# Optimization experiments

Measured on AMD Instinct MI355X. Metric: run time of the kernel, lower is better.

Reference implementation:

```python
import jax, jax.numpy as jnp
import numpy as np


def setup_inputs() -> dict:
    key = jax.random.key(0)
    ks = jax.random.split(key, 10)
    B, L, D_MODEL = 2, 2048, 1024
    D_INNER, N, W, R = 2048, 16, 4, 64
    s = 0.02
    return {
        "hidden_states": jax.random.normal(ks[0], (B, L, D_MODEL), jnp.float32),
        "in_proj_w": jax.random.normal(ks[1], (2 * D_INNER, D_MODEL), jnp.float32) * s,
        "conv_w": jax.random.normal(ks[2], (D_INNER, W), jnp.float32) * 0.2,
        "conv_b": jax.random.normal(ks[3], (D_INNER,), jnp.float32) * 0.02,
        "x_proj_w": jax.random.normal(ks[4], (R + 2 * N, D_INNER), jnp.float32) * s,
        "dt_proj_w": jax.random.normal(ks[5], (D_INNER, R), jnp.float32) * (R ** -0.5),
        "dt_proj_b": jnp.log(jnp.expm1(jnp.exp(jax.random.uniform(ks[6], (D_INNER,), jnp.float32, np.log(1e-3), np.log(1e-1)))) + 1e-20),
        "A_log": jnp.log(jnp.broadcast_to(jnp.arange(1, N + 1, dtype=jnp.float32), (D_INNER, N))),
        "D_param": jnp.ones((D_INNER,), jnp.float32),
        "out_proj_w": jax.random.normal(ks[7], (D_MODEL, D_INNER), jnp.float32) * s,
    }


def _mamba_fwd(hidden_states, in_proj_w, conv_w, conv_b, x_proj_w,
               dt_proj_w, dt_proj_b, A_log, D_param, out_proj_w):
    Bsz, L, _ = hidden_states.shape
    d_inner = conv_w.shape[0]
    n = A_log.shape[1]
    r = dt_proj_w.shape[1]

    # input projection -> x, z  (each [B, L, d_inner])
    xz = jnp.einsum('bld,ed->ble', hidden_states, in_proj_w)
    x, z = xz[..., :d_inner], xz[..., d_inner:]

    # depthwise causal conv over L with SiLU
    x_bdl = jnp.transpose(x, (0, 2, 1))  # [B, d, L]
    kern = conv_w[:, None, :]            # [d, 1, W]
    xc = jax.lax.conv_general_dilated(
        x_bdl, kern, window_strides=(1,), padding=[(conv_w.shape[1] - 1, 0)],
        dimension_numbers=('NCH', 'OIH', 'NCH'), feature_group_count=d_inner)
    xc = xc + conv_b[None, :, None]
    xc = xc * jax.nn.sigmoid(xc)         # silu, [B, d, L]
    u = jnp.transpose(xc, (0, 2, 1))     # [B, L, d]

    # SSM parameter projections
    x_dbl = jnp.einsum('bld,ed->ble', u, x_proj_w)   # [B, L, r+2n]
    dt_lo = x_dbl[..., :r]
    B_ssm = x_dbl[..., r:r + n]                       # [B, L, n]
    C_ssm = x_dbl[..., r + n:]                        # [B, L, n]
    delta = jax.nn.softplus(jnp.einsum('blr,dr->bld', dt_lo, dt_proj_w) + dt_proj_b)

    A = -jnp.exp(A_log)  # [d, n]

    # selective scan over time (sequential recurrence)
    def step(h, inp):
        d_t, u_t, b_t, c_t = inp  # [B,d], [B,d], [B,n], [B,n]
        dA = jnp.exp(d_t[..., None] * A)                       # [B,d,n]
        h = dA * h + (d_t * u_t)[..., None] * b_t[:, None, :]  # [B,d,n]
        y_t = jnp.einsum('bdn,bn->bd', h, c_t)
        return h, y_t

    h0 = jnp.zeros((Bsz, d_inner, n), dtype=u.dtype)
    xs = (jnp.transpose(delta, (1, 0, 2)), jnp.transpose(u, (1, 0, 2)),
          jnp.transpose(B_ssm, (1, 0, 2)), jnp.transpose(C_ssm, (1, 0, 2)))
    _, ys = jax.lax.scan(step, h0, xs)           # ys: [L, B, d]
    y = jnp.transpose(ys, (1, 0, 2)) + u * D_param
    y = y * (z * jax.nn.sigmoid(z))              # gate: y * silu(z)
    return jnp.einsum('bld,ed->ble', y, out_proj_w)


def reference(hidden_states, in_proj_w, conv_w, conv_b, x_proj_w,
              dt_proj_w, dt_proj_b, A_log, D_param, out_proj_w):
    return _mamba_fwd(hidden_states, in_proj_w, conv_w, conv_b, x_proj_w,
                      dt_proj_w, dt_proj_b, A_log, D_param, out_proj_w)
```

## Files before the change

### kernel.cpp

```cpp
#include <hip/hip_runtime.h>
#include <cstdint>
#include <cstddef>

#define Bsz  2
#define Lseq 2048
#define DM   1024
#define DI   2048
#define NS   16
#define RR   64
#define BL   (Bsz * Lseq)
#define TC   64
#define NC   (Lseq / TC)

typedef unsigned short u16;
typedef __attribute__((ext_vector_type(8))) short short8;
typedef __attribute__((ext_vector_type(4))) float f32x4;

__device__ __forceinline__ u16 f32_to_bf16(float f) {
  union { float f; unsigned int u; } v; v.f = f;
  unsigned int lsb = (v.u >> 16) & 1u;
  v.u += 0x7fffu + lsb;
  return (u16)(v.u >> 16);
}
__device__ __forceinline__ float bf16_to_f32(u16 h) {
  union { unsigned int u; float f; } v; v.u = ((unsigned int)h) << 16;
  return v.f;
}

__global__ void cvt_f32_bf16(const float* __restrict__ src, u16* __restrict__ dst, int n) {
  int i = (blockIdx.x * blockDim.x + threadIdx.x) * 4;
  if (i + 4 <= n) {
    float4 v = *(const float4*)(src + i);
    dst[i + 0] = f32_to_bf16(v.x);
    dst[i + 1] = f32_to_bf16(v.y);
    dst[i + 2] = f32_to_bf16(v.z);
    dst[i + 3] = f32_to_bf16(v.w);
  } else {
    for (; i < n; ++i) dst[i] = f32_to_bf16(src[i]);
  }
}

__global__ void split_bf16_kernel(const float* __restrict__ src,
                                  u16* __restrict__ hi, u16* __restrict__ lo, int n) {
  int i = blockIdx.x * blockDim.x + threadIdx.x;
  if (i >= n) return;
  const float v = src[i];
  const u16 h = f32_to_bf16(v);
  hi[i] = h;
  lo[i] = f32_to_bf16(v - bf16_to_f32(h));
}

__global__ void split_dt_kernel(const float* __restrict__ xdbl,
                                u16* __restrict__ hi, u16* __restrict__ lo) {
  int i = blockIdx.x * blockDim.x + threadIdx.x;
  if (i >= BL * 64) return;
  const int m = i >> 6, k = i & 63;
  const float v = xdbl[(size_t)m * 96 + k];
  const u16 h = f32_to_bf16(v);
  hi[i] = h;
  lo[i] = f32_to_bf16(v - bf16_to_f32(h));
}

__device__ __forceinline__ void gload_lds16(const u16* g, u16* l) {
  __builtin_amdgcn_global_load_lds(
      (const __attribute__((address_space(1))) unsigned int*)g,
      (__attribute__((address_space(3))) unsigned int*)l,
      16, 0, 0);
}

__global__ __launch_bounds__(256) void gemm128_bt(
    const u16* __restrict__ A, const u16* __restrict__ Bt,
    float* __restrict__ outA, float* __restrict__ outB,
    int split, int ldA, int ldB, int K)
{
  __shared__ __align__(16) u16 As[128 * 32];
  __shared__ __align__(16) u16 Bs[128 * 32];
  const int tid  = threadIdx.x;
  const int lane = tid & 63;
  const int wid  = tid >> 6;
  const int m0 = blockIdx.y * 128;
  const int n0 = blockIdx.x * 128;
  const int wr = wid >> 1, wc = wid & 1;

  const f32x4 zero = {0.f, 0.f, 0.f, 0.f};
  f32x4 acc[4][4];
#pragma unroll
  for (int i = 0; i < 4; ++i)
#pragma unroll
    for (int j = 0; j < 4; ++j) acc[i][j] = zero;

  const int l16 = lane * 16;

  for (int k0 = 0; k0 < K; k0 += 32) {
    __syncthreads();
#pragma unroll
    for (int c = 0; c < 2; ++c) {
      const int base = c * 4096 + wid * 1024;
      const int ofs  = base + l16;
      const int row  = ofs >> 6;
      const int col  = (ofs >> 1) & 31;
      gload_lds16(A  + (size_t)(m0 + row) * K + k0 + col, (u16*)((char*)As + base));
      gload_lds16(Bt + (size_t)(n0 + row) * K + k0 + col, (u16*)((char*)Bs + base));
    }
    __syncthreads();

    const int kk = (lane >> 4) * 8;
    const int ra = wr * 64 + (lane & 15);
    const int rb = wc * 64 + (lane & 15);
    short8 af[4], bf[4];
#pragma unroll
    for (int i = 0; i < 4; ++i) af[i] = *(const short8*)&As[(ra + i * 16) * 32 + kk];
#pragma unroll
    for (int j = 0; j < 4; ++j) bf[j] = *(const short8*)&Bs[(rb + j * 16) * 32 + kk];
#pragma unroll
    for (int i = 0; i < 4; ++i)
#pragma unroll
      for (int j = 0; j < 4; ++j)
        acc[i][j] = __builtin_amdgcn_mfma_f32_16x16x32_bf16(af[i], bf[j], acc[i][j], 0, 0, 0);
  }

  const int cr = (lane >> 4) * 4;
  const int cc = lane & 15;
#pragma unroll
  for (int i = 0; i < 4; ++i)
#pragma unroll
    for (int j = 0; j < 4; ++j)
#pragma unroll
      for (int r = 0; r < 4; ++r) {
        const int m = m0 + wr * 64 + i * 16 + cr + r;
        const int n = n0 + wc * 64 + j * 16 + cc;
        const float v = acc[i][j][r];
        if (n < split) outA[(size_t)m * ldA + n] = v;
        else           outB[(size_t)m * ldB + (n - split)] = v;
      }
}

__global__ __launch_bounds__(256) void gemm_wave16_bt(
    const u16* __restrict__ A, const u16* __restrict__ Bt,
    float* __restrict__ C, int M, int N, int K)
{
  const int wg   = blockIdx.x * 4 + (threadIdx.x >> 6);
  const int lane = threadIdx.x & 63;
  const int ntiles = N / 16;
  const int mt = wg / ntiles, nt = wg % ntiles;
  if (mt * 16 >= M) return;

  const u16* arow = A  + (size_t)(mt * 16 + (lane & 15)) * K + ((lane >> 4) * 8);
  const u16* brow = Bt + (size_t)(nt * 16 + (lane & 15)) * K + ((lane >> 4) * 8);
  f32x4 acc = {0.f, 0.f, 0.f, 0.f};
  for (int k0 = 0; k0 < K; k0 += 32) {
    short8 a = *(const short8*)(arow + k0);
    short8 b = *(const short8*)(brow + k0);
    acc = __builtin_amdgcn_mfma_f32_16x16x32_bf16(a, b, acc, 0, 0, 0);
  }
  const int cr = (lane >> 4) * 4, cc = lane & 15;
#pragma unroll
  for (int r = 0; r < 4; ++r)
    C[(size_t)(mt * 16 + cr + r) * N + nt * 16 + cc] = acc[r];
}

__global__ __launch_bounds__(256) void dt_gemm_mfma(
    const u16* __restrict__ ahi, const u16* __restrict__ alo,
    const u16* __restrict__ bhi, const u16* __restrict__ blo,
    const float* __restrict__ dtb, float* __restrict__ delta)
{
  const int wg   = blockIdx.x * 4 + (threadIdx.x >> 6);
  const int lane = threadIdx.x & 63;
  const int mt = wg >> 7, nt = wg & 127;

  const size_t aofs = (size_t)(mt * 16 + (lane & 15)) * 64 + ((lane >> 4) * 8);
  const size_t bofs = (size_t)(nt * 16 + (lane & 15)) * 64 + ((lane >> 4) * 8);

  f32x4 acc = {0.f, 0.f, 0.f, 0.f};
#pragma unroll
  for (int k0 = 0; k0 < 64; k0 += 32) {
    const short8 Ah = *(const short8*)(ahi + aofs + k0);
    const short8 Al = *(const short8*)(alo + aofs + k0);
    const short8 Bh = *(const short8*)(bhi + bofs + k0);
    const short8 Bl = *(const short8*)(blo + bofs + k0);
    acc = __builtin_amdgcn_mfma_f32_16x16x32_bf16(Ah, Bh, acc, 0, 0, 0);
    acc = __builtin_amdgcn_mfma_f32_16x16x32_bf16(Ah, Bl, acc, 0, 0, 0);
    acc = __builtin_amdgcn_mfma_f32_16x16x32_bf16(Al, Bh, acc, 0, 0, 0);
  }

  const int cr = (lane >> 4) * 4, cc = lane & 15;
  const int n  = nt * 16 + cc;
  const float b = dtb[n];
#pragma unroll
  for (int r = 0; r < 4; ++r) {
    const float s = acc[r] + b;
    const float sp = fmaxf(s, 0.f) + __logf(1.f + __expf(-fabsf(s)));
    delta[(size_t)(mt * 16 + cr + r) * DI + n] = sp;
  }
}

__global__ void conv_silu_kernel(const float* __restrict__ x,
                                 const float* __restrict__ cw, const float* __restrict__ cb,
                                 float* __restrict__ uf, u16* __restrict__ ub)
{
  const int idx = blockIdx.x * blockDim.x + threadIdx.x;
  if (idx >= BL * DI) return;
  const int d  = idx & (DI - 1);
  const int bl = idx >> 11;
  const int l  = bl & (Lseq - 1);
  const float4 w = *(const float4*)(cw + d * 4);
  float acc = cb[d];
  const float* xp = x + (size_t)bl * DI + d;
  const float x0 = (l >= 3) ? xp[-3 * DI] : 0.f;
  const float x1 = (l >= 2) ? xp[-2 * DI] : 0.f;
  const float x2 = (l >= 1) ? xp[-1 * DI] : 0.f;
  const float x3 = xp[0];
  acc += x0 * w.x + x1 * w.y + x2 * w.z + x3 * w.w;
  const float s = acc / (1.f + __expf(-acc));
  uf[idx] = s;
  ub[idx] = f32_to_bf16(s);
}


__global__ __launch_bounds__(256) void scan_chunk_ps(
    const float* __restrict__ delta, const float* __restrict__ u,
    const float* __restrict__ xdbl, const float* __restrict__ alog,
    float* __restrict__ Pout, float* __restrict__ Sout)
{
  __shared__ float Bl[TC][NS];
  const int b   = blockIdx.z;
  const int c   = blockIdx.y;
  const int d   = blockIdx.x * 256 + threadIdx.x;
  const int tid = threadIdx.x;
  const size_t rowBase = (size_t)b * Lseq + (size_t)c * TC;

  {
    const int row = tid >> 2, c4 = (tid & 3) * 4;
    *(float4*)&Bl[row][c4] = *(const float4*)&xdbl[(rowBase + row) * 96 + RR + c4];
  }
  __syncthreads();

  float A[NS];
#pragma unroll
  for (int n4 = 0; n4 < 4; ++n4) {
    const float4 a4 = *(const float4*)&alog[(size_t)d * NS + n4 * 4];
    A[n4 * 4 + 0] = -__expf(a4.x);
    A[n4 * 4 + 1] = -__expf(a4.y);
    A[n4 * 4 + 2] = -__expf(a4.z);
    A[n4 * 4 + 3] = -__expf(a4.w);
  }

  float h[NS], P[NS];
#pragma unroll
  for (int n = 0; n < NS; ++n) { h[n] = 0.f; P[n] = 1.f; }

#pragma unroll 4
  for (int t = 0; t < TC; ++t) {
    const float dt  = delta[(rowBase + t) * DI + d];
    const float ut  = u[(rowBase + t) * DI + d];
    const float dtu = dt * ut;
#pragma unroll
    for (int n = 0; n < NS; ++n) {
      const float dA = __expf(dt * A[n]);
      P[n] *= dA;
      h[n] = dA * h[n] + dtu * Bl[t][n];
    }
  }

  const size_t base = (size_t)(b * NC + c) * NS * DI + d;
#pragma unroll
  for (int n = 0; n < NS; ++n) {
    Pout[base + (size_t)n * DI] = P[n];
    Sout[base + (size_t)n * DI] = h[n];
  }
}

__global__ __launch_bounds__(256) void scan_combine(
    const float* __restrict__ P, const float* __restrict__ S,
    float* __restrict__ Hin)
{
  const int gid = blockIdx.x * 256 + threadIdx.x;
  const int b   = gid >> 15;
  const int nd  = gid & 32767;
  float h = 0.f;
  for (int c = 0; c < NC; ++c) {
    const size_t o = (size_t)(b * NC + c) * (NS * DI) + nd;
    const float Pc = P[o];
    const float Sc = S[o];
    Hin[o] = h;
    h = Pc * h + Sc;
  }
}

__global__ __launch_bounds__(256) void scan_chunk_y(
    const float* __restrict__ delta, const float* __restrict__ u,
    const float* __restrict__ xdbl, const float* __restrict__ alog,
    const float* __restrict__ dpar, const float* __restrict__ z,
    const float* __restrict__ Hin, u16* __restrict__ yb)
{
  __shared__ float Bl[TC][NS];
  __shared__ float Cl[TC][NS];
  const int b   = blockIdx.z;
  const int c   = blockIdx.y;
  const int d   = blockIdx.x * 256 + threadIdx.x;
  const int tid = threadIdx.x;
  const size_t rowBase = (size_t)b * Lseq + (size_t)c * TC;

  {
    const int row = tid >> 2, c4 = (tid & 3) * 4;
    *(float4*)&Bl[row][c4] = *(const float4*)&xdbl[(rowBase + row) * 96 + RR + c4];
    *(float4*)&Cl[row][c4] = *(const float4*)&xdbl[(rowBase + row) * 96 + RR + NS + c4];
  }
  __syncthreads();

  float A[NS];
#pragma unroll
  for (int n4 = 0; n4 < 4; ++n4) {
    const float4 a4 = *(const float4*)&alog[(size_t)d * NS + n4 * 4];
    A[n4 * 4 + 0] = -__expf(a4.x);
    A[n4 * 4 + 1] = -__expf(a4.y);
    A[n4 * 4 + 2] = -__expf(a4.z);
    A[n4 * 4 + 3] = -__expf(a4.w);
  }
  const float Dv = dpar[d];

  float h[NS];
  const size_t sbase = (size_t)(b * NC + c) * NS * DI + d;
#pragma unroll
  for (int n = 0; n < NS; ++n) h[n] = Hin[sbase + (size_t)n * DI];

#pragma unroll 4
  for (int t = 0; t < TC; ++t) {
    const float dt  = delta[(rowBase + t) * DI + d];
    const float ut  = u[(rowBase + t) * DI + d];
    const float zv  = z[(rowBase + t) * DI + d];
    const float dtu = dt * ut;
    float y = 0.f;
#pragma unroll
    for (int n = 0; n < NS; ++n) {
      const float dA = __expf(dt * A[n]);
      h[n] = dA * h[n] + dtu * Bl[t][n];
      y += h[n] * Cl[t][n];
    }
    const float yv = y + ut * Dv;
    const float g  = zv / (1.f + __expf(-zv));
    yb[(rowBase + t) * DI + d] = f32_to_bf16(yv * g);
  }
}

extern "C" void kernel_launch(void* const* d_in, const int* in_sizes, int n_in,
                              void* d_out, int out_size, void* d_ws, size_t ws_size,
                              hipStream_t stream)
{
  const float* hs   = (const float*)d_in[0];
  const float* win  = (const float*)d_in[1];
  const float* cw   = (const float*)d_in[2];
  const float* cb   = (const float*)d_in[3];
  const float* wxp  = (const float*)d_in[4];
  const float* wdt  = (const float*)d_in[5];
  const float* bdt  = (const float*)d_in[6];
  const float* alog = (const float*)d_in[7];
  const float* dpar = (const float*)d_in[8];
  const float* wout = (const float*)d_in[9];
  float* out = (float*)d_out;

  char* ws = (char*)d_ws;
  size_t off = 0;
  auto alloc = [&](size_t bytes) -> void* {
    void* p = ws + off;
    off += (bytes + 255) & ~(size_t)255;
    return p;
  };
  u16*   hs_b   = (u16*)  alloc((size_t)BL * DM * 2);
  u16*   win_b  = (u16*)  alloc((size_t)2 * DI * DM * 2);
  u16*   wxp_b  = (u16*)  alloc((size_t)96 * DI * 2);
  u16*   wout_b = (u16*)  alloc((size_t)DM * DI * 2);
  float* xbuf   = (float*)alloc((size_t)BL * DI * 4);
  float* zbuf   = (float*)alloc((size_t)BL * DI * 4);
  float* ubuf   = (float*)alloc((size_t)BL * DI * 4);
  u16*   ub16   = (u16*)  alloc((size_t)BL * DI * 2);
  float* xdbl   = (float*)alloc((size_t)BL * 96 * 4);
  float* Pbuf   = (float*)alloc((size_t)Bsz * NC * DI * NS * 4);
  float* Sbuf   = (float*)alloc((size_t)Bsz * NC * DI * NS * 4);
  u16*   dt_hi  = (u16*)  alloc((size_t)BL * 64 * 2);
  u16*   dt_lo  = (u16*)  alloc((size_t)BL * 64 * 2);
  u16*   w_hi   = (u16*)  alloc((size_t)DI * 64 * 2);
  u16*   w_lo   = (u16*)  alloc((size_t)DI * 64 * 2);
  float* deltab = xbuf;
  u16*   y_b    = ub16;
  float* Hin    = Pbuf;

  const int thr = 256;
  cvt_f32_bf16<<<(BL * DM / 4 + thr - 1) / thr, thr, 0, stream>>>(hs, hs_b, BL * DM);
  cvt_f32_bf16<<<(2 * DI * DM / 4 + thr - 1) / thr, thr, 0, stream>>>(win, win_b, 2 * DI * DM);
  cvt_f32_bf16<<<(96 * DI / 4 + thr - 1) / thr, thr, 0, stream>>>(wxp, wxp_b, 96 * DI);
  cvt_f32_bf16<<<(DM * DI / 4 + thr - 1) / thr, thr, 0, stream>>>(wout, wout_b, DM * DI);
  split_bf16_kernel<<<(DI * 64) / thr, thr, 0, stream>>>(wdt, w_hi, w_lo, DI * 64);

  {
    dim3 g(4096 / 128, BL / 128);
    gemm128_bt<<<g, 256, 0, stream>>>(hs_b, win_b, xbuf, zbuf, DI, DI, DI, DM);
  }

  conv_silu_kernel<<<(BL * DI) / 256, 256, 0, stream>>>(xbuf, cw, cb, ubuf, ub16);

  gemm_wave16_bt<<<(BL / 16) * (96 / 16) / 4, 256, 0, stream>>>(ub16, wxp_b, xdbl, BL, 96, DI);

  split_dt_kernel<<<(BL * 64) / thr, thr, 0, stream>>>(xdbl, dt_hi, dt_lo);
  dt_gemm_mfma<<<(256 * 128) / 4, 256, 0, stream>>>(dt_hi, dt_lo, w_hi, w_lo, bdt, deltab);

  {
    dim3 gA(DI / 256, NC, Bsz);
    scan_chunk_ps<<<gA, 256, 0, stream>>>(deltab, ubuf, xdbl, alog, Pbuf, Sbuf);
    scan_combine<<<(Bsz * DI * NS) / 256, 256, 0, stream>>>(Pbuf, Sbuf, Hin);
    scan_chunk_y<<<gA, 256, 0, stream>>>(deltab, ubuf, xdbl, alog, dpar, zbuf, Hin, y_b);
  }

  {
    dim3 g(DM / 128, BL / 128);
    gemm128_bt<<<g, 256, 0, stream>>>(y_b, wout_b, out, out, DM, DM, DM, DI);
  }
}
```

Measured before the change: 294.3 us.

## Store x/z/u intermediates in bf16 and fuse dt split into x_proj GEMM

The input projection GEMM now writes x and z as bf16 instead of fp32. The conv kernel reads bf16 and is vectorised four channels per thread, producing only a bf16 u buffer. Both scan kernels read u and z as bf16. The x_proj GEMM epilogue now does the hi/lo bf16 split for the dt columns, which removes the separate split kernel and a launch. This roughly halves the global traffic for the large BL×DI intermediates, at the cost of lower precision in u, z and the pre-conv x, which may affect accuracy tolerance.

```diff
diff --git a/kernel.cpp b/kernel.cpp
--- a/kernel.cpp
+++ b/kernel.cpp
@@ -13,6 +13,7 @@
 #define NC   (Lseq / TC)
 
 typedef unsigned short u16;
+typedef __attribute__((ext_vector_type(4))) unsigned short u16x4;
 typedef __attribute__((ext_vector_type(8))) short short8;
 typedef __attribute__((ext_vector_type(4))) float f32x4;
 
@@ -50,17 +51,6 @@
   lo[i] = f32_to_bf16(v - bf16_to_f32(h));
 }
 
-__global__ void split_dt_kernel(const float* __restrict__ xdbl,
-                                u16* __restrict__ hi, u16* __restrict__ lo) {
-  int i = blockIdx.x * blockDim.x + threadIdx.x;
-  if (i >= BL * 64) return;
-  const int m = i >> 6, k = i & 63;
-  const float v = xdbl[(size_t)m * 96 + k];
-  const u16 h = f32_to_bf16(v);
-  hi[i] = h;
-  lo[i] = f32_to_bf16(v - bf16_to_f32(h));
-}
-
 __device__ __forceinline__ void gload_lds16(const u16* g, u16* l) {
   __builtin_amdgcn_global_load_lds(
       (const __attribute__((address_space(1))) unsigned int*)g,
@@ -68,9 +58,10 @@
       16, 0, 0);
 }
 
+template<bool BF16OUT>
 __global__ __launch_bounds__(256) void gemm128_bt(
     const u16* __restrict__ A, const u16* __restrict__ Bt,
-    float* __restrict__ outA, float* __restrict__ outB,
+    void* __restrict__ outA_, void* __restrict__ outB_,
     int split, int ldA, int ldB, int K)
 {
   __shared__ __align__(16) u16 As[128 * 32];
@@ -130,33 +121,49 @@
         const int m = m0 + wr * 64 + i * 16 + cr + r;
         const int n = n0 + wc * 64 + j * 16 + cc;
         const float v = acc[i][j][r];
-        if (n < split) outA[(size_t)m * ldA + n] = v;
-        else           outB[(size_t)m * ldB + (n - split)] = v;
+        const bool isA = (n < split);
+        const int  nn  = isA ? n : n - split;
+        const int  ld  = isA ? ldA : ldB;
+        if constexpr (BF16OUT) {
+          u16* o = isA ? (u16*)outA_ : (u16*)outB_;
+          o[(size_t)m * ld + nn] = f32_to_bf16(v);
+        } else {
+          float* o = isA ? (float*)outA_ : (float*)outB_;
+          o[(size_t)m * ld + nn] = v;
+        }
       }
 }
 
-__global__ __launch_bounds__(256) void gemm_wave16_bt(
+__global__ __launch_bounds__(256) void gemm_xproj(
     const u16* __restrict__ A, const u16* __restrict__ Bt,
-    float* __restrict__ C, int M, int N, int K)
+    float* __restrict__ xdbl, u16* __restrict__ dhi, u16* __restrict__ dlo)
 {
   const int wg   = blockIdx.x * 4 + (threadIdx.x >> 6);
   const int lane = threadIdx.x & 63;
-  const int ntiles = N / 16;
-  const int mt = wg / ntiles, nt = wg % ntiles;
-  if (mt * 16 >= M) return;
-
-  const u16* arow = A  + (size_t)(mt * 16 + (lane & 15)) * K + ((lane >> 4) * 8);
-  const u16* brow = Bt + (size_t)(nt * 16 + (lane & 15)) * K + ((lane >> 4) * 8);
+  const int mt = wg / 6, nt = wg % 6;
+
+  const u16* arow = A  + (size_t)(mt * 16 + (lane & 15)) * DI + ((lane >> 4) * 8);
+  const u16* brow = Bt + (size_t)(nt * 16 + (lane & 15)) * DI + ((lane >> 4) * 8);
   f32x4 acc = {0.f, 0.f, 0.f, 0.f};
-  for (int k0 = 0; k0 < K; k0 += 32) {
+  for (int k0 = 0; k0 < DI; k0 += 32) {
     short8 a = *(const short8*)(arow + k0);
     short8 b = *(const short8*)(brow + k0);
     acc = __builtin_amdgcn_mfma_f32_16x16x32_bf16(a, b, acc, 0, 0, 0);
   }
   const int cr = (lane >> 4) * 4, cc = lane & 15;
-#pragma unroll
-  for (int r = 0; r < 4; ++r)
-    C[(size_t)(mt * 16 + cr + r) * N + nt * 16 + cc] = acc[r];
+  const int n  = nt * 16 + cc;
+#pragma unroll
+  for (int r = 0; r < 4; ++r) {
+    const int m = mt * 16 + cr + r;
+    const float v = acc[r];
+    if (n < RR) {
+      const u16 h = f32_to_bf16(v);
+      dhi[(size_t)m * RR + n] = h;
+      dlo[(size_t)m * RR + n] = f32_to_bf16(v - bf16_to_f32(h));
+    } else {
+      xdbl[(size_t)m * 96 + n] = v;
+    }
+  }
 }
 
 __global__ __launch_bounds__(256) void dt_gemm_mfma(
@@ -194,31 +201,38 @@
   }
 }
 
-__global__ void conv_silu_kernel(const float* __restrict__ x,
+__global__ void conv_silu_kernel(const u16* __restrict__ x,
                                  const float* __restrict__ cw, const float* __restrict__ cb,
-                                 float* __restrict__ uf, u16* __restrict__ ub)
-{
-  const int idx = blockIdx.x * blockDim.x + threadIdx.x;
-  if (idx >= BL * DI) return;
-  const int d  = idx & (DI - 1);
-  const int bl = idx >> 11;
+                                 u16* __restrict__ ub)
+{
+  const int idx  = blockIdx.x * blockDim.x + threadIdx.x;
+  const int base = idx * 4;
+  const int d  = base & (DI - 1);
+  const int bl = base >> 11;
   const int l  = bl & (Lseq - 1);
-  const float4 w = *(const float4*)(cw + d * 4);
-  float acc = cb[d];
-  const float* xp = x + (size_t)bl * DI + d;
-  const float x0 = (l >= 3) ? xp[-3 * DI] : 0.f;
-  const float x1 = (l >= 2) ? xp[-2 * DI] : 0.f;
-  const float x2 = (l >= 1) ? xp[-1 * DI] : 0.f;
-  const float x3 = xp[0];
-  acc += x0 * w.x + x1 * w.y + x2 * w.z + x3 * w.w;
-  const float s = acc / (1.f + __expf(-acc));
-  uf[idx] = s;
-  ub[idx] = f32_to_bf16(s);
+  const u16* xp = x + (size_t)bl * DI + d;
+  const u16x4 zv = {0, 0, 0, 0};
+  const u16x4 x3 = *(const u16x4*)xp;
+  const u16x4 x2 = (l >= 1) ? *(const u16x4*)(xp - DI)     : zv;
+  const u16x4 x1 = (l >= 2) ? *(const u16x4*)(xp - 2 * DI) : zv;
+  const u16x4 x0 = (l >= 3) ? *(const u16x4*)(xp - 3 * DI) : zv;
+  const float4 bias = *(const float4*)&cb[d];
+  u16x4 out;
+#pragma unroll
+  for (int j = 0; j < 4; ++j) {
+    const float4 w = *(const float4*)&cw[(d + j) * 4];
+    float acc = ((const float*)&bias)[j];
+    acc += bf16_to_f32(x0[j]) * w.x + bf16_to_f32(x1[j]) * w.y +
+           bf16_to_f32(x2[j]) * w.z + bf16_to_f32(x3[j]) * w.w;
+    const float s = acc / (1.f + __expf(-acc));
+    out[j] = f32_to_bf16(s);
+  }
+  *(u16x4*)(ub + (size_t)bl * DI + d) = out;
 }
 
 
 __global__ __launch_bounds__(256) void scan_chunk_ps(
-    const float* __restrict__ delta, const float* __restrict__ u,
+    const float* __restrict__ delta, const u16* __restrict__ u,
     const float* __restrict__ xdbl, const float* __restrict__ alog,
     float* __restrict__ Pout, float* __restrict__ Sout)
 {
@@ -252,7 +266,7 @@
 #pragma unroll 4
   for (int t = 0; t < TC; ++t) {
     const float dt  = delta[(rowBase + t) * DI + d];
-    const float ut  = u[(rowBase + t) * DI + d];
+    const float ut  = bf16_to_f32(u[(rowBase + t) * DI + d]);
     const float dtu = dt * ut;
 #pragma unroll
     for (int n = 0; n < NS; ++n) {
@@ -288,9 +302,9 @@
 }
 
 __global__ __launch_bounds__(256) void scan_chunk_y(
-    const float* __restrict__ delta, const float* __restrict__ u,
+    const float* __restrict__ delta, const u16* __restrict__ u,
     const float* __restrict__ xdbl, const float* __restrict__ alog,
-    const float* __restrict__ dpar, const float* __restrict__ z,
+    const float* __restrict__ dpar, const u16* __restrict__ z,
     const float* __restrict__ Hin, u16* __restrict__ yb)
 {
   __shared__ float Bl[TC][NS];
@@ -327,8 +341,8 @@
 #pragma unroll 4
   for (int t = 0; t < TC; ++t) {
     const float dt  = delta[(rowBase + t) * DI + d];
-    const float ut  = u[(rowBase + t) * DI + d];
-    const float zv  = z[(rowBase + t) * DI + d];
+    const float ut  = bf16_to_f32(u[(rowBase + t) * DI + d]);
+    const float zv  = bf16_to_f32(z[(rowBase + t) * DI + d]);
     const float dtu = dt * ut;
     float y = 0.f;
 #pragma unroll
@@ -370,10 +384,10 @@
   u16*   win_b  = (u16*)  alloc((size_t)2 * DI * DM * 2);
   u16*   wxp_b  = (u16*)  alloc((size_t)96 * DI * 2);
   u16*   wout_b = (u16*)  alloc((size_t)DM * DI * 2);
-  float* xbuf   = (float*)alloc((size_t)BL * DI * 4);
-  float* zbuf   = (float*)alloc((size_t)BL * DI * 4);
-  float* ubuf   = (float*)alloc((size_t)BL * DI * 4);
+  u16*   xbuf   = (u16*)  alloc((size_t)BL * DI * 2);
+  u16*   zbuf   = (u16*)  alloc((size_t)BL * DI * 2);
   u16*   ub16   = (u16*)  alloc((size_t)BL * DI * 2);
+  float* deltab = (float*)alloc((size_t)BL * DI * 4);
   float* xdbl   = (float*)alloc((size_t)BL * 96 * 4);
   float* Pbuf   = (float*)alloc((size_t)Bsz * NC * DI * NS * 4);
   float* Sbuf   = (float*)alloc((size_t)Bsz * NC * DI * NS * 4);
@@ -381,7 +395,6 @@
   u16*   dt_lo  = (u16*)  alloc((size_t)BL * 64 * 2);
   u16*   w_hi   = (u16*)  alloc((size_t)DI * 64 * 2);
   u16*   w_lo   = (u16*)  alloc((size_t)DI * 64 * 2);
-  float* deltab = xbuf;
   u16*   y_b    = ub16;
   float* Hin    = Pbuf;
 
@@ -394,25 +407,24 @@
 
   {
     dim3 g(4096 / 128, BL / 128);
-    gemm128_bt<<<g, 256, 0, stream>>>(hs_b, win_b, xbuf, zbuf, DI, DI, DI, DM);
-  }
-
-  conv_silu_kernel<<<(BL * DI) / 256, 256, 0, stream>>>(xbuf, cw, cb, ubuf, ub16);
-
-  gemm_wave16_bt<<<(BL / 16) * (96 / 16) / 4, 256, 0, stream>>>(ub16, wxp_b, xdbl, BL, 96, DI);
-
-  split_dt_kernel<<<(BL * 64) / thr, thr, 0, stream>>>(xdbl, dt_hi, dt_lo);
+    gemm128_bt<true><<<g, 256, 0, stream>>>(hs_b, win_b, xbuf, zbuf, DI, DI, DI, DM);
+  }
+
+  conv_silu_kernel<<<(BL * DI / 4) / 256, 256, 0, stream>>>(xbuf, cw, cb, ub16);
+
+  gemm_xproj<<<(256 * 6) / 4, 256, 0, stream>>>(ub16, wxp_b, xdbl, dt_hi, dt_lo);
+
   dt_gemm_mfma<<<(256 * 128) / 4, 256, 0, stream>>>(dt_hi, dt_lo, w_hi, w_lo, bdt, deltab);
 
   {
     dim3 gA(DI / 256, NC, Bsz);
-    scan_chunk_ps<<<gA, 256, 0, stream>>>(deltab, ubuf, xdbl, alog, Pbuf, Sbuf);
+    scan_chunk_ps<<<gA, 256, 0, stream>>>(deltab, ub16, xdbl, alog, Pbuf, Sbuf);
     scan_combine<<<(Bsz * DI * NS) / 256, 256, 0, stream>>>(Pbuf, Sbuf, Hin);
-    scan_chunk_y<<<gA, 256, 0, stream>>>(deltab, ubuf, xdbl, alog, dpar, zbuf, Hin, y_b);
+    scan_chunk_y<<<gA, 256, 0, stream>>>(deltab, ub16, xdbl, alog, dpar, zbuf, Hin, y_b);
   }
 
   {
     dim3 g(DM / 128, BL / 128);
-    gemm128_bt<<<g, 256, 0, stream>>>(y_b, wout_b, out, out, DM, DM, DM, DI);
-  }
-}
+    gemm128_bt<false><<<g, 256, 0, stream>>>(y_b, wout_b, out, out, DM, DM, DM, DI);
+  }
+}
```

Result: no change. 294.1 us (-0.1%).
